# Optimization experiments

Hardware: AMD Instinct MI355X
Metric: run time of the kernel (lower is better)

## Reference

```python
import jax, jax.numpy as jnp
import numpy as np

CUTOFF = 5.0
NUM_RADIAL = 8
MAX_DEGREE = 3
EMB_DIM = 64
N_ELEM = 83
N_EDGES = 400000
NUM_LM = (MAX_DEGREE + 1) ** 2  # 16
# degree of each (l,m) slot: [0, 1,1,1, 2x5, 3x7]
DEG = jnp.asarray([0] + [1] * 3 + [2] * 5 + [3] * 7, dtype=jnp.int32)


def _spherical_harmonics(u):
    """Racah-normalized real spherical harmonics up to l=3 on unit vectors u (N,3).
    Cartesian order for l=1 (x, y, z), standard m=-l..l order otherwise. Returns (N,16)."""
    x, y, z = u[:, 0], u[:, 1], u[:, 2]
    x2, y2, z2 = x * x, y * y, z * z
    s3 = jnp.sqrt(3.0)
    s15 = jnp.sqrt(15.0)
    s5_8 = jnp.sqrt(5.0 / 8.0)
    s3_8 = jnp.sqrt(3.0 / 8.0)
    cols = [
        jnp.ones_like(x),                 # l=0
        x, y, z,                          # l=1 (Cartesian order)
        s3 * x * y,                       # l=2, m=-2
        s3 * y * z,                       # l=2, m=-1
        0.5 * (3.0 * z2 - 1.0),           # l=2, m=0
        s3 * x * z,                       # l=2, m=1
        0.5 * s3 * (x2 - y2),             # l=2, m=2
        s5_8 * y * (3.0 * x2 - y2),       # l=3, m=-3
        s15 * x * y * z,                  # l=3, m=-2
        s3_8 * y * (5.0 * z2 - 1.0),      # l=3, m=-1
        0.5 * z * (5.0 * z2 - 3.0),       # l=3, m=0
        s3_8 * x * (5.0 * z2 - 1.0),      # l=3, m=1
        0.5 * s15 * z * (x2 - y2),        # l=3, m=2
        s5_8 * x * (x2 - 3.0 * y2),       # l=3, m=3
    ]
    return jnp.stack(cols, axis=-1)


def setup_inputs() -> dict:
    key = jax.random.key(0)
    k1, k2, k3, k4, k5 = jax.random.split(key, 5)
    # displacements scaled so |r| spans [0, cutoff] realistically
    neighbour_displacements = jax.random.normal(k1, (N_EDGES, 3), dtype=jnp.float32) * 2.0
    Z_j = jax.random.randint(k2, (N_EDGES,), 0, N_ELEM, dtype=jnp.int32)
    emb_table = jax.random.normal(k3, (N_ELEM, EMB_DIM), dtype=jnp.float32)
    dense_w = jax.random.normal(k4, (EMB_DIM, NUM_RADIAL), dtype=jnp.float32) / jnp.sqrt(float(EMB_DIM))
    dense_b = jnp.zeros((NUM_RADIAL,), dtype=jnp.float32)
    tensor_w = jax.random.normal(k5, (MAX_DEGREE + 1, NUM_RADIAL), dtype=jnp.float32)  # one weight per path (0,l,l)
    return {
        "neighbour_displacements": neighbour_displacements,
        "Z_j": Z_j,
        "emb_table": emb_table,
        "dense_w": dense_w,
        "dense_b": dense_b,
        "tensor_w": tensor_w,
    }


def reference(neighbour_displacements, Z_j, emb_table, dense_w, dense_b, tensor_w):
    d = neighbour_displacements
    r = jnp.linalg.norm(d, axis=-1)                        # (N,)
    r_safe = jnp.where(r > 0.0, r, 1.0)
    u = d / r_safe[:, None]                                # unit vectors (N,3)
    Y = _spherical_harmonics(u)                            # (N,16)
    # sinc radial basis: jnp.sinc(k * r / cutoff), k = 1..num_radial
    k = jnp.arange(1, NUM_RADIAL + 1, dtype=jnp.float32)
    radial = jnp.sinc(r[:, None] * k / CUTOFF)             # (N,8)
    cut = jnp.where(r < CUTOFF, 0.5 * (jnp.cos(jnp.pi * r / CUTOFF) + 1.0), 0.0)
    rb = radial * cut[:, None]                             # (N,8)
    basis = Y[:, :, None] * rb[:, None, :]                 # (N,16,8)
    # species embedding -> dense transform to num_radial channels (scalar feature)
    t = emb_table[Z_j] @ dense_w + dense_b                 # (N,8)
    # CG tensor product: scalar (l=0) x basis (l) -> l, per-path learnable weight
    w_lm = tensor_w[DEG]                                   # (16,8)
    y = t[:, None, :] * basis * w_lm[None]                 # (N,16,8)
    # equivariant swish: y_lm * sigmoid(y_00) (= swish on scalar channel)
    gate = jax.nn.sigmoid(y[:, 0:1, :])
    return y * gate
```

## Files before the change

### kernel.cpp

```cpp
#include <hip/hip_runtime.h>
#include <math.h>

#define NUM_RADIAL 8
#define EMB_DIM    64
#define N_ELEM     83
#define TILE       256

typedef float f4 __attribute__((ext_vector_type(4)));

__global__ void srb_precompute_t(const float* __restrict__ emb,
                                 const float* __restrict__ dw,
                                 const float* __restrict__ db,
                                 float* __restrict__ t_table) {
    int idx = blockIdx.x * blockDim.x + threadIdx.x;
    if (idx >= N_ELEM * NUM_RADIAL) return;
    int z = idx >> 3;
    int k = idx & 7;
    float acc = db[k];
    const float* e = emb + z * EMB_DIM;
    #pragma unroll 8
    for (int j = 0; j < EMB_DIM; ++j)
        acc += e[j] * dw[j * NUM_RADIAL + k];
    t_table[idx] = acc;
}

__global__ __launch_bounds__(256) void srb_main(
    const float* __restrict__ disp,
    const int*   __restrict__ Zj,
    const float* __restrict__ tw,
    const float* __restrict__ t_table,
    float*       __restrict__ out,
    int n_edges)
{
    __shared__ float Yl[TILE * 17];
    __shared__ float CGl[TILE * 12];

    const int tid  = threadIdx.x;
    const int lane = tid & 63;
    const int wv   = tid >> 6;
    const int e    = blockIdx.x * TILE + tid;

    const int jj  = lane & 31;
    const int lm  = jj >> 1;
    const int k0  = (jj & 1) * 4;
    const int l   = (lm > 0) + (lm > 3) + (lm > 8);
    const f4  wl  = *reinterpret_cast<const f4*>(tw + l * NUM_RADIAL + k0);

    if (e < n_edges) {
        const float dx = disp[3 * e + 0];
        const float dy = disp[3 * e + 1];
        const float dz = disp[3 * e + 2];
        const float r2 = dx * dx + dy * dy + dz * dz;
        const float r  = sqrtf(r2);
        const float rinv = (r > 0.0f) ? __builtin_amdgcn_rcpf(r) : 0.0f;
        const float x = dx * rinv, y = dy * rinv, z = dz * rinv;
        const float x2 = x * x, y2 = y * y, z2 = z * z;

        const float s3   = 1.7320508075688772f;
        const float s15  = 3.8729833462074170f;
        const float s5_8 = 0.7905694150420949f;
        const float s3_8 = 0.6123724356957945f;

        float* Yp = &Yl[tid * 17];
        Yp[0]  = 1.0f;
        Yp[1]  = x;
        Yp[2]  = y;
        Yp[3]  = z;
        Yp[4]  = s3 * x * y;
        Yp[5]  = s3 * y * z;
        Yp[6]  = 0.5f * (3.0f * z2 - 1.0f);
        Yp[7]  = s3 * x * z;
        Yp[8]  = 0.5f * s3 * (x2 - y2);
        Yp[9]  = s5_8 * y * (3.0f * x2 - y2);
        Yp[10] = s15 * x * y * z;
        Yp[11] = s3_8 * y * (5.0f * z2 - 1.0f);
        Yp[12] = 0.5f * z * (5.0f * z2 - 3.0f);
        Yp[13] = s3_8 * x * (5.0f * z2 - 1.0f);
        Yp[14] = 0.5f * s15 * z * (x2 - y2);
        Yp[15] = s5_8 * x * (x2 - 3.0f * y2);

        const float PI  = 3.14159265358979323846f;
        const float cut = (r < 5.0f) ? (0.5f * (__cosf(PI * r * 0.2f) + 1.0f))
                                     : 0.0f;
        const float pib = PI * r * 0.2f;

        const int zidx = Zj[e];
        const f4 t0 = *reinterpret_cast<const f4*>(t_table + zidx * NUM_RADIAL);
        const f4 t1 = *reinterpret_cast<const f4*>(t_table + zidx * NUM_RADIAL + 4);
        float t[NUM_RADIAL] = { t0.x, t0.y, t0.z, t0.w, t1.x, t1.y, t1.z, t1.w };

        f4 cga, cgb;
        #pragma unroll
        for (int k = 0; k < NUM_RADIAL; ++k) {
            const float px = pib * (float)(k + 1);
            const float s  = (px != 0.0f) ? (__sinf(px) * __builtin_amdgcn_rcpf(px))
                                          : 1.0f;
            const float c  = t[k] * (s * cut);
            const float y0 = c * tw[k];
            const float gate = __builtin_amdgcn_rcpf(1.0f + __expf(-y0));
            const float cg = c * gate;
            if (k < 4) ((float*)&cga)[k] = cg; else ((float*)&cgb)[k - 4] = cg;
        }
        f4* CGp = reinterpret_cast<f4*>(&CGl[tid * 12]);
        CGp[0] = cga;
        CGp[1] = cgb;
    }

    __asm__ volatile("s_waitcnt lgkmcnt(0)" ::: "memory");
    __builtin_amdgcn_sched_barrier(0);

    const int el0 = wv * 64;
    f4* out4 = reinterpret_cast<f4*>(out);
    #pragma unroll 8
    for (int it = 0; it < 32; ++it) {
        const int el   = el0 + it * 2 + (lane >> 5);
        const int edge = blockIdx.x * TILE + el;
        if (edge < n_edges) {
            const float yv = Yl[el * 17 + lm];
            const f4 cg = *reinterpret_cast<const f4*>(&CGl[el * 12 + k0]);
            const f4 o  = (yv * cg) * wl;
            out4[edge * 32 + jj] = o;
        }
    }
}

extern "C" void kernel_launch(void* const* d_in, const int* in_sizes, int n_in,
                              void* d_out, int out_size, void* d_ws, size_t ws_size,
                              hipStream_t stream) {
    const float* disp = (const float*)d_in[0];
    const int*   Zj   = (const int*)  d_in[1];
    const float* emb  = (const float*)d_in[2];
    const float* dw   = (const float*)d_in[3];
    const float* db   = (const float*)d_in[4];
    const float* tw   = (const float*)d_in[5];
    float* t_table = (float*)d_ws;
    float* out     = (float*)d_out;

    const int n = in_sizes[1];

    hipLaunchKernelGGL(srb_precompute_t, dim3(3), dim3(256), 0, stream,
                       emb, dw, db, t_table);

    const int nblocks = (n + TILE - 1) / TILE;
    hipLaunchKernelGGL(srb_main, dim3(nblocks), dim3(256), 0, stream,
                       disp, Zj, tw, t_table, out, n);
}
```

Before: 42.17 us.

## Fuse species embedding dense transform into main kernel, drop precompute launch

Removes the separate kernel that built the 83x8 t-table and instead computes each edge's 64x8 matvec (embedding row times dense weights) inline in the main kernel. This eliminates one kernel launch and the inter-kernel dependency. In exchange every edge does 512 extra FMAs and reads a 256-byte embedding row plus the dense weights, which adds compute and cache traffic to a kernel that is largely bound by output writes.

```diff
diff --git a/kernel.cpp b/kernel.cpp
--- a/kernel.cpp
+++ b/kernel.cpp
@@ -8,27 +8,13 @@
 
 typedef float f4 __attribute__((ext_vector_type(4)));
 
-__global__ void srb_precompute_t(const float* __restrict__ emb,
-                                 const float* __restrict__ dw,
-                                 const float* __restrict__ db,
-                                 float* __restrict__ t_table) {
-    int idx = blockIdx.x * blockDim.x + threadIdx.x;
-    if (idx >= N_ELEM * NUM_RADIAL) return;
-    int z = idx >> 3;
-    int k = idx & 7;
-    float acc = db[k];
-    const float* e = emb + z * EMB_DIM;
-    #pragma unroll 8
-    for (int j = 0; j < EMB_DIM; ++j)
-        acc += e[j] * dw[j * NUM_RADIAL + k];
-    t_table[idx] = acc;
-}
-
-__global__ __launch_bounds__(256) void srb_main(
+__global__ __launch_bounds__(256) void srb_fused(
     const float* __restrict__ disp,
     const int*   __restrict__ Zj,
+    const float* __restrict__ emb,
+    const float* __restrict__ dw,
+    const float* __restrict__ db,
     const float* __restrict__ tw,
-    const float* __restrict__ t_table,
     float*       __restrict__ out,
     int n_edges)
 {
@@ -79,15 +65,30 @@
         Yp[14] = 0.5f * s15 * z * (x2 - y2);
         Yp[15] = s5_8 * x * (x2 - 3.0f * y2);
 
+        const int zidx = Zj[e];
+        const float* erow = emb + zidx * EMB_DIM;
+        f4 tacc0 = { db[0], db[1], db[2], db[3] };
+        f4 tacc1 = { db[4], db[5], db[6], db[7] };
+        #pragma unroll
+        for (int j4 = 0; j4 < EMB_DIM / 4; ++j4) {
+            const f4 ev = *reinterpret_cast<const f4*>(erow + j4 * 4);
+            #pragma unroll
+            for (int c = 0; c < 4; ++c) {
+                const float ej = ((const float*)&ev)[c];
+                const int   j  = j4 * 4 + c;
+                const f4 w0 = *reinterpret_cast<const f4*>(dw + j * NUM_RADIAL);
+                const f4 w1 = *reinterpret_cast<const f4*>(dw + j * NUM_RADIAL + 4);
+                tacc0 += ej * w0;
+                tacc1 += ej * w1;
+            }
+        }
+        float t[NUM_RADIAL] = { tacc0.x, tacc0.y, tacc0.z, tacc0.w,
+                                tacc1.x, tacc1.y, tacc1.z, tacc1.w };
+
         const float PI  = 3.14159265358979323846f;
         const float cut = (r < 5.0f) ? (0.5f * (__cosf(PI * r * 0.2f) + 1.0f))
                                      : 0.0f;
         const float pib = PI * r * 0.2f;
-
-        const int zidx = Zj[e];
-        const f4 t0 = *reinterpret_cast<const f4*>(t_table + zidx * NUM_RADIAL);
-        const f4 t1 = *reinterpret_cast<const f4*>(t_table + zidx * NUM_RADIAL + 4);
-        float t[NUM_RADIAL] = { t0.x, t0.y, t0.z, t0.w, t1.x, t1.y, t1.z, t1.w };
 
         f4 cga, cgb;
         #pragma unroll
@@ -133,15 +134,11 @@
     const float* dw   = (const float*)d_in[3];
     const float* db   = (const float*)d_in[4];
     const float* tw   = (const float*)d_in[5];
-    float* t_table = (float*)d_ws;
-    float* out     = (float*)d_out;
+    float* out = (float*)d_out;
 
     const int n = in_sizes[1];
 
-    hipLaunchKernelGGL(srb_precompute_t, dim3(3), dim3(256), 0, stream,
-                       emb, dw, db, t_table);
-
     const int nblocks = (n + TILE - 1) / TILE;
-    hipLaunchKernelGGL(srb_main, dim3(nblocks), dim3(256), 0, stream,
-                       disp, Zj, tw, t_table, out, n);
+    hipLaunchKernelGGL(srb_fused, dim3(nblocks), dim3(256), 0, stream,
+                       disp, Zj, emb, dw, db, tw, out, n);
 }
```

After: 43.91 us. +4.1%, slower.

## Make main kernel persistent with double-buffered LDS and prefetch of next tile

Applied to the files above, without the earlier changes.

Swaps the one-block-per-tile launch for a fixed grid of 512 persistent blocks that loop over tiles with a grid stride. Each wave double-buffers its LDS staging, prefetching the next tile's displacements and species indices and computing it while storing the current tile's output. The intent is to hide input-load latency and avoid launching many short blocks. The cost is LDS that doubles to about 58KB per block, which with launch_bounds(256,2) may limit occupancy, plus a capped grid that may underuse the GPU on a write-bound kernel.

```diff
diff --git a/kernel.cpp b/kernel.cpp
--- a/kernel.cpp
+++ b/kernel.cpp
@@ -5,6 +5,7 @@
 #define EMB_DIM    64
 #define N_ELEM     83
 #define TILE       256
+#define NBLOCKS    512
 
 typedef float f4 __attribute__((ext_vector_type(4)));
 
@@ -24,21 +25,20 @@
     t_table[idx] = acc;
 }
 
-__global__ __launch_bounds__(256) void srb_main(
+__global__ __launch_bounds__(256, 2) void srb_main(
     const float* __restrict__ disp,
     const int*   __restrict__ Zj,
     const float* __restrict__ tw,
     const float* __restrict__ t_table,
     float*       __restrict__ out,
-    int n_edges)
+    int n_edges, int ntiles)
 {
-    __shared__ float Yl[TILE * 17];
-    __shared__ float CGl[TILE * 12];
+    __shared__ float Yl[2 * 4 * 64 * 17];
+    __shared__ float CGl[2 * 4 * 64 * 12];
 
     const int tid  = threadIdx.x;
     const int lane = tid & 63;
     const int wv   = tid >> 6;
-    const int e    = blockIdx.x * TILE + tid;
 
     const int jj  = lane & 31;
     const int lm  = jj >> 1;
@@ -46,10 +46,20 @@
     const int l   = (lm > 0) + (lm > 3) + (lm > 8);
     const f4  wl  = *reinterpret_cast<const f4*>(tw + l * NUM_RADIAL + k0);
 
-    if (e < n_edges) {
-        const float dx = disp[3 * e + 0];
-        const float dy = disp[3 * e + 1];
-        const float dz = disp[3 * e + 2];
+    f4* out4 = reinterpret_cast<f4*>(out);
+    const int stride = gridDim.x;
+
+    auto loadA = [&](int T, float& dxo, float& dyo, float& dzo, int& zo) {
+        const int e = T * TILE + wv * 64 + lane;
+        if (e < n_edges) {
+            dxo = disp[3 * e + 0];
+            dyo = disp[3 * e + 1];
+            dzo = disp[3 * e + 2];
+            zo  = Zj[e];
+        } else { dxo = 0.0f; dyo = 0.0f; dzo = 0.0f; zo = 0; }
+    };
+
+    auto compute = [&](int buf, float dx, float dy, float dz, f4 t0, f4 t1) {
         const float r2 = dx * dx + dy * dy + dz * dz;
         const float r  = sqrtf(r2);
         const float rinv = (r > 0.0f) ? __builtin_amdgcn_rcpf(r) : 0.0f;
@@ -61,7 +71,7 @@
         const float s5_8 = 0.7905694150420949f;
         const float s3_8 = 0.6123724356957945f;
 
-        float* Yp = &Yl[tid * 17];
+        float* Yp = &Yl[(buf * 4 + wv) * (64 * 17) + lane * 17];
         Yp[0]  = 1.0f;
         Yp[1]  = x;
         Yp[2]  = y;
@@ -84,9 +94,6 @@
                                      : 0.0f;
         const float pib = PI * r * 0.2f;
 
-        const int zidx = Zj[e];
-        const f4 t0 = *reinterpret_cast<const f4*>(t_table + zidx * NUM_RADIAL);
-        const f4 t1 = *reinterpret_cast<const f4*>(t_table + zidx * NUM_RADIAL + 4);
         float t[NUM_RADIAL] = { t0.x, t0.y, t0.z, t0.w, t1.x, t1.y, t1.z, t1.w };
 
         f4 cga, cgb;
@@ -101,27 +108,67 @@
             const float cg = c * gate;
             if (k < 4) ((float*)&cga)[k] = cg; else ((float*)&cgb)[k - 4] = cg;
         }
-        f4* CGp = reinterpret_cast<f4*>(&CGl[tid * 12]);
+        f4* CGp = reinterpret_cast<f4*>(
+            &CGl[(buf * 4 + wv) * (64 * 12) + lane * 12]);
         CGp[0] = cga;
         CGp[1] = cgb;
-    }
+    };
 
+    auto stores = [&](int T, int buf) {
+        const int ebase  = T * TILE + wv * 64;
+        const int ybase  = (buf * 4 + wv) * (64 * 17);
+        const int cgbase = (buf * 4 + wv) * (64 * 12);
+        #pragma unroll 8
+        for (int it = 0; it < 32; ++it) {
+            const int el   = it * 2 + (lane >> 5);
+            const int edge = ebase + el;
+            if (edge < n_edges) {
+                const float yv = Yl[ybase + el * 17 + lm];
+                const f4 cg = *reinterpret_cast<const f4*>(&CGl[cgbase + el * 12 + k0]);
+                out4[edge * 32 + jj] = (yv * cg) * wl;
+            }
+        }
+    };
+
+    int T = blockIdx.x;
+    if (T >= ntiles) return;
+
+    float dxA, dyA, dzA; int zA;
+    loadA(T, dxA, dyA, dzA, zA);
+    const f4 t0A = *reinterpret_cast<const f4*>(t_table + zA * NUM_RADIAL);
+    const f4 t1A = *reinterpret_cast<const f4*>(t_table + zA * NUM_RADIAL + 4);
+
+    int  Tn   = T + stride;
+    bool more = (Tn < ntiles);
+    float dxB = 0.0f, dyB = 0.0f, dzB = 0.0f; int zB = 0;
+    if (more) loadA(Tn, dxB, dyB, dzB, zB);
+
+    compute(0, dxA, dyA, dzA, t0A, t1A);
     __asm__ volatile("s_waitcnt lgkmcnt(0)" ::: "memory");
     __builtin_amdgcn_sched_barrier(0);
 
-    const int el0 = wv * 64;
-    f4* out4 = reinterpret_cast<f4*>(out);
-    #pragma unroll 8
-    for (int it = 0; it < 32; ++it) {
-        const int el   = el0 + it * 2 + (lane >> 5);
-        const int edge = blockIdx.x * TILE + el;
-        if (edge < n_edges) {
-            const float yv = Yl[el * 17 + lm];
-            const f4 cg = *reinterpret_cast<const f4*>(&CGl[el * 12 + k0]);
-            const f4 o  = (yv * cg) * wl;
-            out4[edge * 32 + jj] = o;
-        }
+    int cur = 0;
+    while (more) {
+        const int  T2    = Tn + stride;
+        const bool more2 = (T2 < ntiles);
+        float dxC = 0.0f, dyC = 0.0f, dzC = 0.0f; int zC = 0;
+        if (more2) loadA(T2, dxC, dyC, dzC, zC);
+        const f4 t0B = *reinterpret_cast<const f4*>(t_table + zB * NUM_RADIAL);
+        const f4 t1B = *reinterpret_cast<const f4*>(t_table + zB * NUM_RADIAL + 4);
+
+        stores(T, cur);
+
+        compute(cur ^ 1, dxB, dyB, dzB, t0B, t1B);
+        __asm__ volatile("s_waitcnt lgkmcnt(0)" ::: "memory");
+        __builtin_amdgcn_sched_barrier(0);
+
+        T = Tn; Tn = T2;
+        dxB = dxC; dyB = dyC; dzB = dzC; zB = zC;
+        more = more2;
+        cur ^= 1;
     }
+
+    stores(T, cur);
 }
 
 extern "C" void kernel_launch(void* const* d_in, const int* in_sizes, int n_in,
@@ -141,7 +188,8 @@
     hipLaunchKernelGGL(srb_precompute_t, dim3(3), dim3(256), 0, stream,
                        emb, dw, db, t_table);
 
-    const int nblocks = (n + TILE - 1) / TILE;
-    hipLaunchKernelGGL(srb_main, dim3(nblocks), dim3(256), 0, stream,
-                       disp, Zj, tw, t_table, out, n);
+    const int ntiles = (n + TILE - 1) / TILE;
+    const int nb = (ntiles < NBLOCKS) ? ntiles : NBLOCKS;
+    hipLaunchKernelGGL(srb_main, dim3(nb), dim3(256), 0, stream,
+                       disp, Zj, tw, t_table, out, n, ntiles);
 }
```

Measured after the change: 42.98 us. About the same (+1.9%).
